# Kernel tuning notes

Hardware: AMD Instinct MI355X
Metric: run time of the kernel (lower is better)

## Reference

```python
import jax, jax.numpy as jnp
import numpy as np
from jax import lax

DOWNSAMPLE = 4.0   # downsample_rate
THRESHOLD = 0.7    # score threshold
NMS_RANGE = 3      # maxpool NMS kernel


def setup_inputs() -> dict:
    key = jax.random.key(0)
    k1, k2 = jax.random.split(key)
    radiace_factor = jax.random.uniform(k1, (8, 80, 192, 192), dtype=jnp.float32)  # class heatmap
    box = jax.random.uniform(k2, (8, 4, 192, 192), dtype=jnp.float32)              # [dx, dy, w, h]
    return {"radiace_factor": radiace_factor, "box": box}


def _nms(heat, kernel):
    # max_pool2d(kernel, stride=1, padding=(kernel-1)//2) == SAME window max
    hmax = lax.reduce_window(heat, -jnp.inf, lax.max,
                             (1, 1, kernel, kernel), (1, 1, 1, 1), 'SAME')
    return heat * (hmax == heat).astype(heat.dtype)


def reference(radiace_factor, box):
    B, C, H, W = radiace_factor.shape
    r = jnp.float32(DOWNSAMPLE)

    heat = _nms(radiace_factor, NMS_RANGE)
    score = heat.max(axis=1)               # [B,H,W] max over categories
    mask = score > THRESHOLD               # [B,H,W] kept peaks

    # grid of (x=col, y=row) matching torch.where(inds)[::-1]
    gx, gy = jnp.meshgrid(jnp.arange(W, dtype=jnp.float32),
                          jnp.arange(H, dtype=jnp.float32), indexing='xy')
    grid = jnp.stack([gx, gy], axis=-1)    # [H,W,2]

    b = jnp.moveaxis(box, 1, -1)           # [B,H,W,4] = (dx,dy,w,h)
    center_xy = (grid + b[..., 0:2]) * r   # [B,H,W,2]
    wh = b[..., 2:4] * r

    lim = jnp.array([W * DOWNSAMPLE, H * DOWNSAMPLE], dtype=jnp.float32)
    x1y1 = jnp.clip(center_xy - wh * 0.5, 0.0, lim)
    x2y2 = jnp.clip(center_xy + wh * 0.5, 0.0, lim)
    boxes = jnp.concatenate([x1y1, x2y2 - x1y1], axis=-1)  # [B,H,W,4] (x1,y1,w,h)

    # Dense, jit-friendly equivalent of the per-batch gather: zero-out non-kept
    m = mask[..., None]
    boxes_kept = jnp.where(m, boxes, 0.0)
    scores_kept = jnp.where(mask, score, 0.0)
    center_kept = jnp.where(m, center_xy, 0.0)
    return boxes_kept, mask, scores_kept, center_kept
```

## Files before the change

### kernel.cpp

```cpp
#include <hip/hip_runtime.h>
#include <math.h>


#define BB 8
#define CC 80
#define HH 192
#define WW 192
#define SS 8
#define NBPIX (BB*HH*WW)

__global__ __launch_bounds__(256) void score_kernel(const float* __restrict__ heat,
                                                    float* __restrict__ part) {
    const int tid  = threadIdx.x;
    const int lane = tid & 63;
    const int wv   = tid >> 6;
    const int yt   = blockIdx.x;
    const int zs   = blockIdx.y;
    const int b    = blockIdx.z;
    const int y0   = yt * SS;
    const bool lok = lane < 48;
    const int  col0 = lane * 4;

    __shared__ float red[4][SS][WW];

    float4 sc[SS];
#pragma unroll
    for (int i = 0; i < SS; ++i) sc[i] = make_float4(0.f, 0.f, 0.f, 0.f);

    const int cbase = (zs * 4 + wv) * 10;
    const float NI = -INFINITY;

    for (int k = 0; k < 10; ++k) {
        const int c = cbase + k;
        const float* hp = heat + ((size_t)(b * CC + c) * HH) * WW;
        float4 v[SS + 2];
#pragma unroll
        for (int r = 0; r < SS + 2; ++r) {
            const int  row = y0 - 1 + r;
            const bool ok  = lok && ((unsigned)row < HH);
            v[r] = ok ? *reinterpret_cast<const float4*>(hp + row * WW + col0)
                      : make_float4(NI, NI, NI, NI);
        }
#pragma unroll
        for (int i = 0; i < SS; ++i) {
            const float4 a = v[i], m = v[i + 1], d = v[i + 2];
            float4 vm;
            vm.x = fmaxf(fmaxf(a.x, m.x), d.x);
            vm.y = fmaxf(fmaxf(a.y, m.y), d.y);
            vm.z = fmaxf(fmaxf(a.z, m.z), d.z);
            vm.w = fmaxf(fmaxf(a.w, m.w), d.w);

            float L = __shfl_up(vm.w, 1);
            float R = __shfl_down(vm.x, 1);
            if (lane == 0)  L = NI;
            if (lane >= 47) R = NI;

            float4 hm;
            hm.x = fmaxf(fmaxf(L,    vm.x), vm.y);
            hm.y = fmaxf(fmaxf(vm.x, vm.y), vm.z);
            hm.z = fmaxf(fmaxf(vm.y, vm.z), vm.w);
            hm.w = fmaxf(fmaxf(vm.z, vm.w), R);

            sc[i].x = fmaxf(sc[i].x, (m.x == hm.x) ? m.x : 0.0f);
            sc[i].y = fmaxf(sc[i].y, (m.y == hm.y) ? m.y : 0.0f);
            sc[i].z = fmaxf(sc[i].z, (m.z == hm.z) ? m.z : 0.0f);
            sc[i].w = fmaxf(sc[i].w, (m.w == hm.w) ? m.w : 0.0f);
        }
    }

    if (lok) {
#pragma unroll
        for (int i = 0; i < SS; ++i)
            *reinterpret_cast<float4*>(&red[wv][i][col0]) = sc[i];
    }
    __syncthreads();

    float* pp = part + ((size_t)(zs * BB + b) * HH + y0) * WW;
#pragma unroll
    for (int k = 0; k < SS * WW / 256; ++k) {
        const int idx = k * 256 + tid;
        const int row = idx / WW, col = idx - row * WW;
        const float mx = fmaxf(fmaxf(red[0][row][col], red[1][row][col]),
                               fmaxf(red[2][row][col], red[3][row][col]));
        pp[idx] = mx;
    }
}

__global__ __launch_bounds__(256) void decode_kernel(const float* __restrict__ box,
                                                     const float* __restrict__ part,
                                                     float* __restrict__ out) {
    const int pix = blockIdx.x * 256 + threadIdx.x;
    if (pix >= NBPIX) return;

    const int b   = pix / (HH * WW);
    const int rem = pix - b * (HH * WW);
    const int y   = rem / WW;
    const int x   = rem - y * WW;

    float* boxes  = out;
    float* maskp  = out + (size_t)4 * NBPIX;
    float* scorep = out + (size_t)5 * NBPIX;
    float* ctr    = out + (size_t)6 * NBPIX;

    const float s = fmaxf(part[pix], part[NBPIX + pix]);
    const bool  m = s > 0.7f;

    const float* bp = box + (size_t)b * 4 * HH * WW + rem;
    const float dx = bp[0];
    const float dy = bp[(size_t)HH * WW];
    const float bw = bp[(size_t)2 * HH * WW];
    const float bh = bp[(size_t)3 * HH * WW];

    const float cx = ((float)x + dx) * 4.0f;
    const float cy = ((float)y + dy) * 4.0f;
    const float w4 = bw * 4.0f;
    const float h4 = bh * 4.0f;
    const float lim = 768.0f;
    const float x1 = fminf(fmaxf(cx - w4 * 0.5f, 0.0f), lim);
    const float y1 = fminf(fmaxf(cy - h4 * 0.5f, 0.0f), lim);
    const float x2 = fminf(fmaxf(cx + w4 * 0.5f, 0.0f), lim);
    const float y2 = fminf(fmaxf(cy + h4 * 0.5f, 0.0f), lim);

    float4 bo;
    bo.x = m ? x1 : 0.0f;
    bo.y = m ? y1 : 0.0f;
    bo.z = m ? (x2 - x1) : 0.0f;
    bo.w = m ? (y2 - y1) : 0.0f;
    reinterpret_cast<float4*>(boxes)[pix] = bo;

    maskp[pix]  = m ? 1.0f : 0.0f;
    scorep[pix] = m ? s : 0.0f;

    float2 cc;
    cc.x = m ? cx : 0.0f;
    cc.y = m ? cy : 0.0f;
    reinterpret_cast<float2*>(ctr)[pix] = cc;
}

extern "C" void kernel_launch(void* const* d_in, const int* in_sizes, int n_in,
                              void* d_out, int out_size, void* d_ws, size_t ws_size,
                              hipStream_t stream) {
    const float* heat = (const float*)d_in[0];
    const float* box  = (const float*)d_in[1];
    float* out  = (float*)d_out;
    float* part = (float*)d_ws;

    dim3 g1(HH / SS, 2, BB);
    score_kernel<<<g1, 256, 0, stream>>>(heat, part);

    decode_kernel<<<NBPIX / 256, 256, 0, stream>>>(box, part, out);
}
```

Measured before the change: 148.3 us.

## Fuse score reduction and box decode into a single kernel

Merges the NMS/score kernel with the decode kernel. Each block now reduces over all 80 channels (20 per wave) and writes the final boxes, mask, scores and centers directly. This removes the intermediate partial-score workspace round trip and a second launch. In exchange, the grid is halved to 192 blocks, each doing twice the serial channel loop, which reduces parallelism on a 256-CU device.

```diff
diff --git a/kernel.cpp b/kernel.cpp
--- a/kernel.cpp
+++ b/kernel.cpp
@@ -7,16 +7,17 @@
 #define HH 192
 #define WW 192
 #define SS 8
-#define NBPIX (BB*HH*WW)
+#define NB (HH*WW)
+#define NBPIX (BB*NB)
 
-__global__ __launch_bounds__(256) void score_kernel(const float* __restrict__ heat,
-                                                    float* __restrict__ part) {
+__global__ __launch_bounds__(256) void fused_kernel(const float* __restrict__ heat,
+                                                    const float* __restrict__ box,
+                                                    float* __restrict__ out) {
     const int tid  = threadIdx.x;
     const int lane = tid & 63;
     const int wv   = tid >> 6;
     const int yt   = blockIdx.x;
-    const int zs   = blockIdx.y;
-    const int b    = blockIdx.z;
+    const int b    = blockIdx.y;
     const int y0   = yt * SS;
     const bool lok = lane < 48;
     const int  col0 = lane * 4;
@@ -27,11 +28,10 @@
 #pragma unroll
     for (int i = 0; i < SS; ++i) sc[i] = make_float4(0.f, 0.f, 0.f, 0.f);
 
-    const int cbase = (zs * 4 + wv) * 10;
     const float NI = -INFINITY;
 
-    for (int k = 0; k < 10; ++k) {
-        const int c = cbase + k;
+    for (int k = 0; k < 20; ++k) {
+        const int c = wv * 20 + k;
         const float* hp = heat + ((size_t)(b * CC + c) * HH) * WW;
         float4 v[SS + 2];
 #pragma unroll
@@ -75,66 +75,54 @@
     }
     __syncthreads();
 
-    float* pp = part + ((size_t)(zs * BB + b) * HH + y0) * WW;
-#pragma unroll
-    for (int k = 0; k < SS * WW / 256; ++k) {
-        const int idx = k * 256 + tid;
-        const int row = idx / WW, col = idx - row * WW;
-        const float mx = fmaxf(fmaxf(red[0][row][col], red[1][row][col]),
-                               fmaxf(red[2][row][col], red[3][row][col]));
-        pp[idx] = mx;
-    }
-}
-
-__global__ __launch_bounds__(256) void decode_kernel(const float* __restrict__ box,
-                                                     const float* __restrict__ part,
-                                                     float* __restrict__ out) {
-    const int pix = blockIdx.x * 256 + threadIdx.x;
-    if (pix >= NBPIX) return;
-
-    const int b   = pix / (HH * WW);
-    const int rem = pix - b * (HH * WW);
-    const int y   = rem / WW;
-    const int x   = rem - y * WW;
-
     float* boxes  = out;
     float* maskp  = out + (size_t)4 * NBPIX;
     float* scorep = out + (size_t)5 * NBPIX;
     float* ctr    = out + (size_t)6 * NBPIX;
 
-    const float s = fmaxf(part[pix], part[NBPIX + pix]);
-    const bool  m = s > 0.7f;
+#pragma unroll
+    for (int k = 0; k < SS * WW / 256; ++k) {
+        const int idx = k * 256 + tid;
+        const int row = idx / WW, col = idx - row * WW;
+        const float s = fmaxf(fmaxf(red[0][row][col], red[1][row][col]),
+                              fmaxf(red[2][row][col], red[3][row][col]));
+        const bool  m = s > 0.7f;
 
-    const float* bp = box + (size_t)b * 4 * HH * WW + rem;
-    const float dx = bp[0];
-    const float dy = bp[(size_t)HH * WW];
-    const float bw = bp[(size_t)2 * HH * WW];
-    const float bh = bp[(size_t)3 * HH * WW];
+        const int y   = y0 + row;
+        const int rem = y * WW + col;
+        const int pix = b * NB + rem;
 
-    const float cx = ((float)x + dx) * 4.0f;
-    const float cy = ((float)y + dy) * 4.0f;
-    const float w4 = bw * 4.0f;
-    const float h4 = bh * 4.0f;
-    const float lim = 768.0f;
-    const float x1 = fminf(fmaxf(cx - w4 * 0.5f, 0.0f), lim);
-    const float y1 = fminf(fmaxf(cy - h4 * 0.5f, 0.0f), lim);
-    const float x2 = fminf(fmaxf(cx + w4 * 0.5f, 0.0f), lim);
-    const float y2 = fminf(fmaxf(cy + h4 * 0.5f, 0.0f), lim);
+        const float* bp = box + (size_t)b * 4 * NB + rem;
+        const float dx = bp[0];
+        const float dy = bp[NB];
+        const float bw = bp[2 * NB];
+        const float bh = bp[3 * NB];
 
-    float4 bo;
-    bo.x = m ? x1 : 0.0f;
-    bo.y = m ? y1 : 0.0f;
-    bo.z = m ? (x2 - x1) : 0.0f;
-    bo.w = m ? (y2 - y1) : 0.0f;
-    reinterpret_cast<float4*>(boxes)[pix] = bo;
+        const float cx = ((float)col + dx) * 4.0f;
+        const float cy = ((float)y   + dy) * 4.0f;
+        const float w4 = bw * 4.0f;
+        const float h4 = bh * 4.0f;
+        const float lim = 768.0f;
+        const float x1 = fminf(fmaxf(cx - w4 * 0.5f, 0.0f), lim);
+        const float y1 = fminf(fmaxf(cy - h4 * 0.5f, 0.0f), lim);
+        const float x2 = fminf(fmaxf(cx + w4 * 0.5f, 0.0f), lim);
+        const float y2 = fminf(fmaxf(cy + h4 * 0.5f, 0.0f), lim);
 
-    maskp[pix]  = m ? 1.0f : 0.0f;
-    scorep[pix] = m ? s : 0.0f;
+        float4 bo;
+        bo.x = m ? x1 : 0.0f;
+        bo.y = m ? y1 : 0.0f;
+        bo.z = m ? (x2 - x1) : 0.0f;
+        bo.w = m ? (y2 - y1) : 0.0f;
+        reinterpret_cast<float4*>(boxes)[pix] = bo;
 
-    float2 cc;
-    cc.x = m ? cx : 0.0f;
-    cc.y = m ? cy : 0.0f;
-    reinterpret_cast<float2*>(ctr)[pix] = cc;
+        maskp[pix]  = m ? 1.0f : 0.0f;
+        scorep[pix] = m ? s : 0.0f;
+
+        float2 cc;
+        cc.x = m ? cx : 0.0f;
+        cc.y = m ? cy : 0.0f;
+        reinterpret_cast<float2*>(ctr)[pix] = cc;
+    }
 }
 
 extern "C" void kernel_launch(void* const* d_in, const int* in_sizes, int n_in,
@@ -142,11 +130,8 @@
                               hipStream_t stream) {
     const float* heat = (const float*)d_in[0];
     const float* box  = (const float*)d_in[1];
-    float* out  = (float*)d_out;
-    float* part = (float*)d_ws;
+    float* out = (float*)d_out;
 
-    dim3 g1(HH / SS, 2, BB);
-    score_kernel<<<g1, 256, 0, stream>>>(heat, part);
-
-    decode_kernel<<<NBPIX / 256, 256, 0, stream>>>(box, part, out);
+    dim3 g(HH / SS, BB);
+    fused_kernel<<<g, 256, 0, stream>>>(heat, box, out);
 }
```

Result: slower. 152.1 us (+2.6%).
